# Optimization experiments

Hardware: AMD Instinct MI355X
Metric: run time of the kernel (lower is better)

The kernel has to match this reference:

```python
import jax, jax.numpy as jnp
import numpy as np

H = 1024        # hidden_size
NH = 16         # num_heads
HD = H // NH    # head_dim
NS = 3          # num_strata


def setup_inputs() -> dict:
    key = jax.random.key(0)
    ks = jax.random.split(key, 12)
    s = 1.0 / np.sqrt(H)
    inp = {
        "hidden_states": jax.random.normal(ks[0], (2, 2048, H), dtype=jnp.float32),
        "Wq": jax.random.uniform(ks[1], (H, H), minval=-s, maxval=s, dtype=jnp.float32),
        "bq": jax.random.uniform(ks[2], (H,), minval=-s, maxval=s, dtype=jnp.float32),
        "Wk": jax.random.uniform(ks[3], (H, H), minval=-s, maxval=s, dtype=jnp.float32),
        "bk": jax.random.uniform(ks[4], (H,), minval=-s, maxval=s, dtype=jnp.float32),
        "Wv": jax.random.uniform(ks[5], (H, H), minval=-s, maxval=s, dtype=jnp.float32),
        "bv": jax.random.uniform(ks[6], (H,), minval=-s, maxval=s, dtype=jnp.float32),
        "Ws": jax.random.uniform(ks[7], (NS, H, H), minval=-s, maxval=s, dtype=jnp.float32),
        "bs": jax.random.uniform(ks[8], (NS, H), minval=-s, maxval=s, dtype=jnp.float32),
        "Wo": jax.random.uniform(ks[9], (H, H), minval=-s, maxval=s, dtype=jnp.float32),
        "bo": jax.random.uniform(ks[10], (H,), minval=-s, maxval=s, dtype=jnp.float32),
    }
    return inp


def reference(hidden_states, Wq, bq, Wk, bk, Wv, bv, Ws, bs, Wo, bo):
    B, S, _ = hidden_states.shape
    # torch nn.Linear: y = x @ W.T + b
    q = hidden_states @ Wq.T + bq
    k = hidden_states @ Wk.T + bk
    v = hidden_states @ Wv.T + bv
    # [B, NH, S, HD]
    q = q.reshape(B, S, NH, HD).transpose(0, 2, 1, 3)
    k = k.reshape(B, S, NH, HD).transpose(0, 2, 1, 3)
    v = v.reshape(B, S, NH, HD).transpose(0, 2, 1, 3)
    scores = jnp.einsum('bhqd,bhkd->bhqk', q, k) / jnp.sqrt(jnp.float32(HD))
    attn = jax.nn.softmax(scores, axis=-1)
    out = jnp.einsum('bhqk,bhkd->bhqd', attn, v)
    attn_output = out.transpose(0, 2, 1, 3).reshape(B, S, H)
    # stratum projections, averaged: [NS, B, S, H] -> mean over strata
    strata = jnp.einsum('bsh,ngh->nbsg', attn_output, Ws) + bs[:, None, None, :]
    enhanced = strata.mean(axis=0)
    output = enhanced @ Wo.T + bo
    return output
```

## Files before the change

### kernel.cpp

```cpp
#include <hip/hip_runtime.h>
#include <stdint.h>

typedef __attribute__((ext_vector_type(8))) short short8;
typedef __attribute__((ext_vector_type(4))) short short4v;
typedef __attribute__((ext_vector_type(4))) float f32x4;
typedef __attribute__((ext_vector_type(16))) float f32x16;
typedef __attribute__((ext_vector_type(2))) unsigned int u32x2;
typedef unsigned int u32;
typedef const __attribute__((address_space(1))) u32* gas_ptr;
typedef __attribute__((address_space(3))) u32* las_ptr;

#define QSCALE 0.18033688011112042f

__device__ inline short f2bf(float x) {
    u32 u = __float_as_uint(x);
    u = u + 0x7FFFu + ((u >> 16) & 1u);
    return (short)(u >> 16);
}
__device__ inline void gload16(const void* g, const void* l) {
    __builtin_amdgcn_global_load_lds((gas_ptr)g, (las_ptr)l, 16, 0, 0);
}

__global__ __launch_bounds__(256) void prep(const float* __restrict__ X,
                                            const float* __restrict__ Wq,
                                            const float* __restrict__ Wk,
                                            const float* __restrict__ Wv,
                                            const float* __restrict__ Wo,
                                            const float* __restrict__ Ws,
                                            const float* __restrict__ bs,
                                            const float* __restrict__ bo,
                                            short* __restrict__ Xb,
                                            short* __restrict__ Wcat,
                                            short* __restrict__ Wob,
                                            short* __restrict__ WmT,
                                            float* __restrict__ bc) {
    __shared__ short T[64][65];
    const int tid = threadIdx.x;
    const int bid = blockIdx.x;
    if (bid < 8192) {
        const float* src;
        short* dst;
        int rel;
        if (bid < 4096)      { src = X;  dst = Xb;                rel = bid; }
        else if (bid < 5120) { src = Wq; dst = Wcat;              rel = bid - 4096; }
        else if (bid < 6144) { src = Wk; dst = Wcat + (1 << 20);  rel = bid - 5120; }
        else if (bid < 7168) { src = Wv; dst = Wcat + (2 << 20);  rel = bid - 6144; }
        else                 { src = Wo; dst = Wob;               rel = bid - 7168; }
        int i = (rel * 256 + tid) * 4;
        float4 v = *(const float4*)&src[i];
        short4v o;
        o[0] = f2bf(v.x); o[1] = f2bf(v.y); o[2] = f2bf(v.z); o[3] = f2bf(v.w);
        *(short4v*)&dst[i] = o;
    } else if (bid < 8448) {
        const int id = bid - 8192;
        const int gx = (id & 15) * 64, jy = (id >> 4) * 64;
        const int HH = 1 << 20;
        for (int e = tid; e < 4096; e += 256) {
            int j = e >> 6, g = e & 63;
            int idx = (jy + j) * 1024 + gx + g;
            float v = (Ws[idx] + Ws[idx + HH] + Ws[idx + 2 * HH]) * (1.0f / 3.0f);
            T[g][j] = f2bf(v);
        }
        __syncthreads();
        for (int e = tid; e < 4096; e += 256) {
            int g = e >> 6, j = e & 63;
            WmT[(long)(gx + g) * 1024 + jy + j] = T[g][j];
        }
    } else {
        const int lane = tid & 63;
        const int n = (bid - 8448) * 4 + (tid >> 6);
        float acc = 0.0f;
        for (int j0 = 0; j0 < 1024; j0 += 64) {
            int j = j0 + lane;
            float bm = (bs[j] + bs[j + 1024] + bs[j + 2048]) * (1.0f / 3.0f);
            acc += Wo[(long)n * 1024 + j] * bm;
        }
#pragma unroll
        for (int off = 1; off < 64; off <<= 1) acc += __shfl_xor(acc, off, 64);
        if (lane == 0) bc[n] = acc + bo[n];
    }
}

__global__ __launch_bounds__(256) void gemm_qkvwc(const short* __restrict__ Xb,
                                                  const short* __restrict__ Wcat,
                                                  const short* __restrict__ Wob,
                                                  const short* __restrict__ WmT,
                                                  const float* __restrict__ bq,
                                                  const float* __restrict__ bk,
                                                  const float* __restrict__ bv,
                                                  short* __restrict__ Qb,
                                                  short* __restrict__ Kb,
                                                  short* __restrict__ Vt,
                                                  short* __restrict__ Wc) {
    __shared__ short As[64 * 64];
    __shared__ short Bs[128 * 64];
    const int K = 1024;
    const int tid  = threadIdx.x;
    const int lane = tid & 63;
    const int wave = tid >> 6;
    const int quad = lane >> 4;
    const int l16  = lane & 15;
    const int bid = blockIdx.x;
    const short *A, *W;
    int m0, n0, sel;
    if (bid < 1536) {
        sel = bid >> 9;
        int r = bid & 511;
        m0 = (r >> 3) * 64;
        n0 = (r & 7) * 128;
        A = Xb;
        W = Wcat + (long)sel * (1 << 20);
    } else {
        int w = bid - 1536;
        sel = 3;
        m0 = (w >> 3) * 64;
        n0 = (w & 7) * 128;
        A = Wob;
        W = WmT;
    }
    const int wm = (wave >> 1) * 32;
    const int wn = (wave & 1) * 64;

    f32x4 acc[2][4] = {};
    const int sr = tid >> 3;
    const int scol = (((tid & 7) ^ (sr & 7)) << 3);
    const int fo_a = ((quad ^ (l16 & 7)) << 3);
    const int fo_b = (((4 + quad) ^ (l16 & 7)) << 3);

    for (int k0 = 0; k0 < K; k0 += 64) {
#pragma unroll
        for (int i = 0; i < 2; i++) {
            int r = i * 32 + sr;
            gload16(&A[(long)(m0 + r) * K + k0 + scol], &As[i * 2048 + wave * 512]);
        }
#pragma unroll
        for (int i = 0; i < 4; i++) {
            int r = i * 32 + sr;
            gload16(&W[(long)(n0 + r) * K + k0 + scol], &Bs[i * 2048 + wave * 512]);
        }
        __syncthreads();
        short8 bfr[4][2];
#pragma unroll
        for (int ni = 0; ni < 4; ni++) {
            const int row = wn + ni * 16 + l16;
            bfr[ni][0] = *(short8*)&Bs[row * 64 + fo_a];
            bfr[ni][1] = *(short8*)&Bs[row * 64 + fo_b];
        }
#pragma unroll
        for (int mi = 0; mi < 2; mi++) {
            const int row = wm + mi * 16 + l16;
            short8 af0 = *(short8*)&As[row * 64 + fo_a];
            short8 af1 = *(short8*)&As[row * 64 + fo_b];
#pragma unroll
            for (int ni = 0; ni < 4; ni++) {
                acc[mi][ni] = __builtin_amdgcn_mfma_f32_16x16x32_bf16(af0, bfr[ni][0],
                                                                      acc[mi][ni], 0, 0, 0);
                acc[mi][ni] = __builtin_amdgcn_mfma_f32_16x16x32_bf16(af1, bfr[ni][1],
                                                                      acc[mi][ni], 0, 0, 0);
            }
        }
        __syncthreads();
    }

#pragma unroll
    for (int mi = 0; mi < 2; mi++) {
#pragma unroll
        for (int ni = 0; ni < 4; ni++) {
            const int n = n0 + wn + ni * 16 + l16;
            const int mbase = m0 + wm + mi * 16 + quad * 4;
            float bv2 = 0.0f;
            if (sel == 0) bv2 = bq[n];
            else if (sel == 1) bv2 = bk[n];
            else if (sel == 2) bv2 = bv[n];
            if (sel == 2) {
                short4v pk;
#pragma unroll
                for (int r = 0; r < 4; r++) pk[r] = f2bf(acc[mi][ni][r] + bv2);
                long addr = ((long)(mbase >> 11) << 21) + (long)n * 2048 + (mbase & 2047);
                *(short4v*)&Vt[addr] = pk;
            } else if (sel == 0) {
#pragma unroll
                for (int r = 0; r < 4; r++)
                    Qb[(long)(mbase + r) * 1024 + n] = f2bf((acc[mi][ni][r] + bv2) * QSCALE);
            } else {
                short* C = (sel == 1) ? Kb : Wc;
#pragma unroll
                for (int r = 0; r < 4; r++)
                    C[(long)(mbase + r) * 1024 + n] = f2bf(acc[mi][ni][r] + bv2);
            }
        }
    }
}

__global__ __launch_bounds__(256) void attn_kernel(const short* __restrict__ Q,
                                                   const short* __restrict__ Kb,
                                                   const short* __restrict__ Vt,
                                                   short* __restrict__ O) {
    __shared__ short Ks[2][64 * 64];
    __shared__ short Vs[64 * 64];
    __shared__ short Ps[4][32 * 64];
    const int tid  = threadIdx.x;
    const int lane = tid & 63;
    const int wave = tid >> 6;
    const int l32  = lane & 31;
    const int hi   = lane >> 5;
    const int sw   = l32 & 7;
    const int q0 = blockIdx.x * 128;
    const int h  = blockIdx.y;
    const int b  = blockIdx.z;

    short8 qB[4];
    {
        const long qbase = (long)(b * 2048 + q0 + wave * 32 + l32) * 1024 + h * 64 + hi * 8;
#pragma unroll
        for (int t = 0; t < 4; t++) qB[t] = *(const short8*)&Q[qbase + t * 16];
    }

    const int sr = tid >> 3;
    const int scol = (((tid & 7) ^ (sr & 7)) << 3);
    const short* Kp = Kb + (long)(b * 2048) * 1024 + h * 64;
    const short* Vp = Vt + ((long)b << 21) + (long)h * 64 * 2048;

    f32x16 o[2] = {};
    float lsum = 0.0f;
    short* const psw = &Ps[wave][0];

#pragma unroll
    for (int i = 0; i < 2; i++) {
        int r = i * 32 + sr;
        gload16(&Kp[(long)r * 1024 + scol], &Ks[0][i * 2048 + wave * 512]);
    }
    __syncthreads();

    for (int kt = 0; kt < 32; kt++) {
        const int cur = kt & 1;
        const int kb = kt * 64;

#pragma unroll
        for (int i = 0; i < 2; i++) {
            int r = i * 32 + sr;
            gload16(&Vp[(long)r * 2048 + kb + scol], &Vs[i * 2048 + wave * 512]);
        }

#pragma unroll
        for (int kvt = 0; kvt < 2; kvt++) {
            const int row = kvt * 32 + l32;
            f32x16 st = {};
#pragma unroll
            for (int step = 0; step < 4; step++) {
                short8 ak = *(short8*)&Ks[cur][row * 64 + (((step * 2 + hi) ^ sw) << 3)];
                st = __builtin_amdgcn_mfma_f32_32x32x16_bf16(ak, qB[step], st, 0, 0, 0);
            }
#pragma unroll
            for (int g = 0; g < 4; g++) {
                float p0 = __builtin_amdgcn_exp2f(st[g * 4 + 0]);
                float p1 = __builtin_amdgcn_exp2f(st[g * 4 + 1]);
                float p2 = __builtin_amdgcn_exp2f(st[g * 4 + 2]);
                float p3 = __builtin_amdgcn_exp2f(st[g * 4 + 3]);
                lsum += (p0 + p1) + (p2 + p3);
                u32 a0 = __float_as_uint(p0) + 0x8000u;
                u32 a1 = __float_as_uint(p1) + 0x8000u;
                u32 a2 = __float_as_uint(p2) + 0x8000u;
                u32 a3 = __float_as_uint(p3) + 0x8000u;
                u32x2 w;
                w[0] = __builtin_amdgcn_perm(a1, a0, 0x07060302u);
                w[1] = __builtin_amdgcn_perm(a3, a2, 0x07060302u);
                *(u32x2*)((char*)psw + l32 * 128 + (((kvt * 4 + g) ^ sw) << 4) + hi * 8) = w;
            }
        }

        short8 pB[4];
#pragma unroll
        for (int step = 0; step < 4; step++)
            pB[step] = *(short8*)&psw[l32 * 64 + (((step * 2 + hi) ^ sw) << 3)];

        __syncthreads();

        if (kt < 31) {
            const int kbn = kb + 64;
#pragma unroll
            for (int i = 0; i < 2; i++) {
                int r = i * 32 + sr;
                gload16(&Kp[(long)(kbn + r) * 1024 + scol],
                        &Ks[cur ^ 1][i * 2048 + wave * 512]);
            }
        }

#pragma unroll
        for (int dt = 0; dt < 2; dt++) {
            const int row = dt * 32 + l32;
#pragma unroll
            for (int step = 0; step < 4; step++) {
                short8 av = *(short8*)&Vs[row * 64 + (((step * 2 + hi) ^ sw) << 3)];
                o[dt] = __builtin_amdgcn_mfma_f32_32x32x16_bf16(av, pB[step], o[dt], 0, 0, 0);
            }
        }

        __syncthreads();
    }

    lsum += __shfl_xor(lsum, 32, 64);
    const float inv = 1.0f / lsum;
    const long rbase = (long)(b * 2048 + q0 + wave * 32 + l32) * 1024 + h * 64;
#pragma unroll
    for (int dt = 0; dt < 2; dt++) {
#pragma unroll
        for (int g = 0; g < 4; g++) {
            short4v pk;
#pragma unroll
            for (int i = 0; i < 4; i++) pk[i] = f2bf(o[dt][g * 4 + i] * inv);
            *(short4v*)&O[rbase + dt * 32 + g * 8 + hi * 4] = pk;
        }
    }
}

__global__ __launch_bounds__(256) void gemm_final(const short* __restrict__ A,
                                                  const short* __restrict__ W,
                                                  const float* __restrict__ bias,
                                                  float* __restrict__ C) {
    __shared__ short As[64 * 64];
    __shared__ short Bs[128 * 64];
    const int K = 1024;
    const int tid  = threadIdx.x;
    const int lane = tid & 63;
    const int wave = tid >> 6;
    const int quad = lane >> 4;
    const int l16  = lane & 15;
    const int bid = blockIdx.x;
    const int m0 = (bid >> 3) * 64;
    const int n0 = (bid & 7) * 128;
    const int wm = (wave >> 1) * 32;
    const int wn = (wave & 1) * 64;

    f32x4 acc[2][4] = {};
    const int sr = tid >> 3;
    const int scol = (((tid & 7) ^ (sr & 7)) << 3);
    const int fo_a = ((quad ^ (l16 & 7)) << 3);
    const int fo_b = (((4 + quad) ^ (l16 & 7)) << 3);

    for (int k0 = 0; k0 < K; k0 += 64) {
#pragma unroll
        for (int i = 0; i < 2; i++) {
            int r = i * 32 + sr;
            gload16(&A[(long)(m0 + r) * K + k0 + scol], &As[i * 2048 + wave * 512]);
        }
#pragma unroll
        for (int i = 0; i < 4; i++) {
            int r = i * 32 + sr;
            gload16(&W[(long)(n0 + r) * K + k0 + scol], &Bs[i * 2048 + wave * 512]);
        }
        __syncthreads();
        short8 bfr[4][2];
#pragma unroll
        for (int ni = 0; ni < 4; ni++) {
            const int row = wn + ni * 16 + l16;
            bfr[ni][0] = *(short8*)&Bs[row * 64 + fo_a];
            bfr[ni][1] = *(short8*)&Bs[row * 64 + fo_b];
        }
#pragma unroll
        for (int mi = 0; mi < 2; mi++) {
            const int row = wm + mi * 16 + l16;
            short8 af0 = *(short8*)&As[row * 64 + fo_a];
            short8 af1 = *(short8*)&As[row * 64 + fo_b];
#pragma unroll
            for (int ni = 0; ni < 4; ni++) {
                acc[mi][ni] = __builtin_amdgcn_mfma_f32_16x16x32_bf16(af0, bfr[ni][0],
                                                                      acc[mi][ni], 0, 0, 0);
                acc[mi][ni] = __builtin_amdgcn_mfma_f32_16x16x32_bf16(af1, bfr[ni][1],
                                                                      acc[mi][ni], 0, 0, 0);
            }
        }
        __syncthreads();
    }

#pragma unroll
    for (int mi = 0; mi < 2; mi++) {
#pragma unroll
        for (int ni = 0; ni < 4; ni++) {
            const int n = n0 + wn + ni * 16 + l16;
            const float bv = bias[n];
            const int mbase = m0 + wm + mi * 16 + quad * 4;
#pragma unroll
            for (int r = 0; r < 4; r++)
                C[(long)(mbase + r) * 1024 + n] = acc[mi][ni][r] + bv;
        }
    }
}

extern "C" void kernel_launch(void* const* d_in, const int* in_sizes, int n_in,
                              void* d_out, int out_size, void* d_ws, size_t ws_size,
                              hipStream_t stream) {
    const float* X  = (const float*)d_in[0];
    const float* Wq = (const float*)d_in[1];
    const float* bq = (const float*)d_in[2];
    const float* Wk = (const float*)d_in[3];
    const float* bk = (const float*)d_in[4];
    const float* Wv = (const float*)d_in[5];
    const float* bv = (const float*)d_in[6];
    const float* Ws = (const float*)d_in[7];
    const float* bs = (const float*)d_in[8];
    const float* Wo = (const float*)d_in[9];
    const float* bo = (const float*)d_in[10];

    char* ws = (char*)d_ws;
    const long MB = 1 << 20;
    short* Xb   = (short*)(ws + 0 * MB);
    short* Wcat = (short*)(ws + 8 * MB);
    short* WmT  = (short*)(ws + 14 * MB);
    short* Wob  = (short*)(ws + 16 * MB);
    short* Wc   = (short*)(ws + 18 * MB);
    float* bc   = (float*)(ws + 20 * MB);
    short* Qb   = (short*)(ws + 21 * MB);
    short* Kbf  = (short*)(ws + 29 * MB);
    short* Vtb  = (short*)(ws + 37 * MB);
    short* AO   = Xb;

    dim3 bb(256);

    prep<<<dim3(8704), bb, 0, stream>>>(X, Wq, Wk, Wv, Wo, Ws, bs, bo,
                                        Xb, Wcat, Wob, WmT, bc);
    gemm_qkvwc<<<dim3(1664), bb, 0, stream>>>(Xb, Wcat, Wob, WmT, bq, bk, bv,
                                              Qb, Kbf, Vtb, Wc);
    attn_kernel<<<dim3(16, 16, 2), bb, 0, stream>>>(Qb, Kbf, Vtb, AO);
    gemm_final<<<dim3(512), bb, 0, stream>>>(AO, Wc, bc, (float*)d_out);
}
```

Before: 229.6 us.

## Split attention KV range across two wave groups and pass P through permlane swaps

Each attention block now runs 512 threads in two groups of four waves. Each group processes half of the key/value sequence, and the partial outputs and row sums are merged through shared memory at the end. The softmax probabilities are packed to bf16 with v_cvt_pk_bf16_f32 and moved into MFMA operand layout with permlane32_swap instead of a round trip through shared memory. This doubles the number of waves in flight per block and drops the LDS writes and reads for P, at the cost of a final reduction step and more shared memory per block.

```diff
diff --git a/kernel.cpp b/kernel.cpp
--- a/kernel.cpp
+++ b/kernel.cpp
@@ -6,6 +6,7 @@
 typedef __attribute__((ext_vector_type(4))) float f32x4;
 typedef __attribute__((ext_vector_type(16))) float f32x16;
 typedef __attribute__((ext_vector_type(2))) unsigned int u32x2;
+typedef __attribute__((ext_vector_type(4))) unsigned int u32x4;
 typedef unsigned int u32;
 typedef const __attribute__((address_space(1))) u32* gas_ptr;
 typedef __attribute__((address_space(3))) u32* las_ptr;
@@ -192,63 +193,65 @@
     }
 }
 
-__global__ __launch_bounds__(256) void attn_kernel(const short* __restrict__ Q,
-                                                   const short* __restrict__ Kb,
-                                                   const short* __restrict__ Vt,
-                                                   short* __restrict__ O) {
-    __shared__ short Ks[2][64 * 64];
-    __shared__ short Vs[64 * 64];
-    __shared__ short Ps[4][32 * 64];
-    const int tid  = threadIdx.x;
-    const int lane = tid & 63;
-    const int wave = tid >> 6;
-    const int l32  = lane & 31;
-    const int hi   = lane >> 5;
-    const int sw   = l32 & 7;
+__global__ __launch_bounds__(512, 4) void attn_kernel(const short* __restrict__ Q,
+                                                      const short* __restrict__ Kb,
+                                                      const short* __restrict__ Vt,
+                                                      short* __restrict__ O) {
+    __shared__ short Ks[2][2][64 * 64];
+    __shared__ short Vs[2][64 * 64];
+    const int tid   = threadIdx.x;
+    const int lane  = tid & 63;
+    const int wave  = tid >> 6;
+    const int group = wave >> 2;
+    const int wv    = wave & 3;
+    const int gtid  = tid & 255;
+    const int l32   = lane & 31;
+    const int hi    = lane >> 5;
+    const int sw    = l32 & 7;
     const int q0 = blockIdx.x * 128;
     const int h  = blockIdx.y;
     const int b  = blockIdx.z;
 
     short8 qB[4];
     {
-        const long qbase = (long)(b * 2048 + q0 + wave * 32 + l32) * 1024 + h * 64 + hi * 8;
+        const long qbase = (long)(b * 2048 + q0 + wv * 32 + l32) * 1024 + h * 64 + hi * 8;
 #pragma unroll
         for (int t = 0; t < 4; t++) qB[t] = *(const short8*)&Q[qbase + t * 16];
     }
 
-    const int sr = tid >> 3;
-    const int scol = (((tid & 7) ^ (sr & 7)) << 3);
-    const short* Kp = Kb + (long)(b * 2048) * 1024 + h * 64;
-    const short* Vp = Vt + ((long)b << 21) + (long)h * 64 * 2048;
+    const int sr = gtid >> 3;
+    const int scol = (((gtid & 7) ^ (sr & 7)) << 3);
+    const short* Kp = Kb + (long)(b * 2048 + group * 1024) * 1024 + h * 64;
+    const short* Vp = Vt + ((long)b << 21) + (long)h * 64 * 2048 + group * 1024;
 
     f32x16 o[2] = {};
     float lsum = 0.0f;
-    short* const psw = &Ps[wave][0];
 
 #pragma unroll
     for (int i = 0; i < 2; i++) {
         int r = i * 32 + sr;
-        gload16(&Kp[(long)r * 1024 + scol], &Ks[0][i * 2048 + wave * 512]);
+        gload16(&Kp[(long)r * 1024 + scol], &Ks[group][0][i * 2048 + wv * 512]);
     }
     __syncthreads();
 
-    for (int kt = 0; kt < 32; kt++) {
+    for (int kt = 0; kt < 16; kt++) {
         const int cur = kt & 1;
         const int kb = kt * 64;
 
 #pragma unroll
         for (int i = 0; i < 2; i++) {
             int r = i * 32 + sr;
-            gload16(&Vp[(long)r * 2048 + kb + scol], &Vs[i * 2048 + wave * 512]);
-        }
-
+            gload16(&Vp[(long)r * 2048 + kb + scol], &Vs[group][i * 2048 + wv * 512]);
+        }
+
+        u32 c0[8], c1[8];
 #pragma unroll
         for (int kvt = 0; kvt < 2; kvt++) {
             const int row = kvt * 32 + l32;
             f32x16 st = {};
 #pragma unroll
             for (int step = 0; step < 4; step++) {
-                short8 ak = *(short8*)&Ks[cur][row * 64 + (((step * 2 + hi) ^ sw) << 3)];
+                short8 ak = *(short8*)&Ks[group][cur][row * 64 + (((step * 2 + hi) ^ sw) << 3)];
                 st = __builtin_amdgcn_mfma_f32_32x32x16_bf16(ak, qB[step], st, 0, 0, 0);
             }
 #pragma unroll
@@ -258,41 +261,43 @@
                 float p2 = __builtin_amdgcn_exp2f(st[g * 4 + 2]);
                 float p3 = __builtin_amdgcn_exp2f(st[g * 4 + 3]);
                 lsum += (p0 + p1) + (p2 + p3);
-                u32 a0 = __float_as_uint(p0) + 0x8000u;
-                u32 a1 = __float_as_uint(p1) + 0x8000u;
-                u32 a2 = __float_as_uint(p2) + 0x8000u;
-                u32 a3 = __float_as_uint(p3) + 0x8000u;
-                u32x2 w;
-                w[0] = __builtin_amdgcn_perm(a1, a0, 0x07060302u);
-                w[1] = __builtin_amdgcn_perm(a3, a2, 0x07060302u);
-                *(u32x2*)((char*)psw + l32 * 128 + (((kvt * 4 + g) ^ sw) << 4) + hi * 8) = w;
-            }
-        }
-
-        short8 pB[4];
-#pragma unroll
-        for (int step = 0; step < 4; step++)
-            pB[step] = *(short8*)&psw[l32 * 64 + (((step * 2 + hi) ^ sw) << 3)];
-
-        __syncthreads();
-
-        if (kt < 31) {
+                u32 w0, w1;
+                asm("v_cvt_pk_bf16_f32 %0, %1, %2" : "=v"(w0) : "v"(p0), "v"(p1));
+                asm("v_cvt_pk_bf16_f32 %0, %1, %2" : "=v"(w1) : "v"(p2), "v"(p3));
+                c0[kvt * 4 + g] = w0;
+                c1[kvt * 4 + g] = w1;
+            }
+        }
+
+        __syncthreads();
+
+        if (kt < 15) {
             const int kbn = kb + 64;
 #pragma unroll
             for (int i = 0; i < 2; i++) {
                 int r = i * 32 + sr;
                 gload16(&Kp[(long)(kbn + r) * 1024 + scol],
-                        &Ks[cur ^ 1][i * 2048 + wave * 512]);
-            }
+                        &Ks[group][cur ^ 1][i * 2048 + wv * 512]);
+            }
+        }
+
+        short8 pB[4];
+#pragma unroll
+        for (int s = 0; s < 4; s++) {
+            u32x2 r0 = __builtin_amdgcn_permlane32_swap(c0[2 * s], c0[2 * s + 1], false, false);
+            u32x2 r1 = __builtin_amdgcn_permlane32_swap(c1[2 * s], c1[2 * s + 1], false, false);
+            u32x4 bw;
+            bw[0] = r0[0]; bw[1] = r1[0]; bw[2] = r0[1]; bw[3] = r1[1];
+            pB[s] = __builtin_bit_cast(short8, bw);
         }
 
 #pragma unroll
         for (int dt = 0; dt < 2; dt++) {
             const int row = dt * 32 + l32;
 #pragma unroll
-            for (int step = 0; step < 4; step++) {
-                short8 av = *(short8*)&Vs[row * 64 + (((step * 2 + hi) ^ sw) << 3)];
-                o[dt] = __builtin_amdgcn_mfma_f32_32x32x16_bf16(av, pB[step], o[dt], 0, 0, 0);
+            for (int s = 0; s < 4; s++) {
+                short8 av = *(short8*)&Vs[group][row * 64 + (((s * 2 + hi) ^ sw) << 3)];
+                o[dt] = __builtin_amdgcn_mfma_f32_32x32x16_bf16(av, pB[s], o[dt], 0, 0, 0);
             }
         }
 
@@ -300,16 +305,36 @@
     }
 
     lsum += __shfl_xor(lsum, 32, 64);
-    const float inv = 1.0f / lsum;
-    const long rbase = (long)(b * 2048 + q0 + wave * 32 + l32) * 1024 + h * 64;
-#pragma unroll
-    for (int dt = 0; dt < 2; dt++) {
-#pragma unroll
-        for (int g = 0; g < 4; g++) {
-            short4v pk;
-#pragma unroll
-            for (int i = 0; i < 4; i++) pk[i] = f2bf(o[dt][g * 4 + i] * inv);
-            *(short4v*)&O[rbase + dt * 32 + g * 8 + hi * 4] = pk;
+    float* cb = (float*)&Ks[0][0][0];
+    float* lb = (float*)&Vs[0][0];
+    const int ql = wv * 32 + l32;
+    if (group == 1) {
+#pragma unroll
+        for (int dt = 0; dt < 2; dt++) {
+#pragma unroll
+            for (int g = 0; g < 4; g++) {
+                f32x4 v4;
+#pragma unroll
+                for (int i = 0; i < 4; i++) v4[i] = o[dt][g * 4 + i];
+                *(f32x4*)&cb[ql * 64 + dt * 32 + g * 8 + hi * 4] = v4;
+            }
+        }
+        if (hi == 0) lb[ql] = lsum;
+    }
+    __syncthreads();
+    if (group == 0) {
+        const float inv = 1.0f / (lsum + lb[ql]);
+        const long rbase = (long)(b * 2048 + q0 + ql) * 1024 + h * 64;
+#pragma unroll
+        for (int dt = 0; dt < 2; dt++) {
+#pragma unroll
+            for (int g = 0; g < 4; g++) {
+                const f32x4 pv = *(const f32x4*)&cb[ql * 64 + dt * 32 + g * 8 + hi * 4];
+                short4v pk;
+#pragma unroll
+                for (int i = 0; i < 4; i++) pk[i] = f2bf((o[dt][g * 4 + i] + pv[i]) * inv);
+                *(short4v*)&O[rbase + dt * 32 + g * 8 + hi * 4] = pk;
+            }
         }
     }
 }
@@ -421,6 +446,6 @@
                                         Xb, Wcat, Wob, WmT, bc);
     gemm_qkvwc<<<dim3(1664), bb, 0, stream>>>(Xb, Wcat, Wob, WmT, bq, bk, bv,
                                               Qb, Kbf, Vtb, Wc);
-    attn_kernel<<<dim3(16, 16, 2), bb, 0, stream>>>(Qb, Kbf, Vtb, AO);
+    attn_kernel<<<dim3(16, 16, 2), dim3(512), 0, stream>>>(Qb, Kbf, Vtb, AO);
     gemm_final<<<dim3(512), bb, 0, stream>>>(AO, Wc, bc, (float*)d_out);
 }
```

Measured after the change: 208.7 us. -9.1%, faster.
